# Optimization experiments

Measured on AMD Instinct MI355X. Metric: run time of the kernel, lower is better.

## Reference

```python
import jax, jax.numpy as jnp
import numpy as np

N_NODES = 100000
N_EDGES = 3200000
NUM_FEATURES = 512
LATENT_DIM = 64
HIDDEN = 2 * LATENT_DIM


def gcn_conv(x, src, dst, deg_inv_sqrt, W, b, n_nodes):
    # GCNConv: out = D^{-1/2} (A+I) D^{-1/2} X W + b  (transform first, then aggregate)
    h = x @ W  # [N, out]
    norm = deg_inv_sqrt[src] * deg_inv_sqrt[dst]  # [E]
    msg = h[src] * norm[:, None]  # gather + scale
    out = jax.ops.segment_sum(msg, dst, num_segments=n_nodes)
    return out + b


def setup_inputs() -> dict:
    key = jax.random.key(0)
    ks = jax.random.split(key, 8)
    features = jax.random.normal(ks[0], (N_NODES, NUM_FEATURES), dtype=jnp.float32)
    edge_index = jax.random.randint(ks[1], (2, N_EDGES), 0, N_NODES, dtype=jnp.int64)
    # Glorot-ish params
    W1 = jax.random.normal(ks[2], (NUM_FEATURES, HIDDEN), dtype=jnp.float32) / np.sqrt(NUM_FEATURES)
    b1 = jnp.zeros((HIDDEN,), dtype=jnp.float32)
    Wm = jax.random.normal(ks[3], (HIDDEN, LATENT_DIM), dtype=jnp.float32) / np.sqrt(HIDDEN)
    bm = jnp.zeros((LATENT_DIM,), dtype=jnp.float32)
    Wv = jax.random.normal(ks[4], (HIDDEN, LATENT_DIM), dtype=jnp.float32) / np.sqrt(HIDDEN)
    bv = jnp.zeros((LATENT_DIM,), dtype=jnp.float32)
    return {"features": features, "edge_index": edge_index,
            "W1": W1, "b1": b1, "Wm": Wm, "bm": bm, "Wv": Wv, "bv": bv}


def reference(features, edge_index, W1, b1, Wm, bm, Wv, bv):
    n = features.shape[0]
    loop = jnp.arange(n, dtype=edge_index.dtype)
    src = jnp.concatenate([edge_index[0], loop])  # add self-loops
    dst = jnp.concatenate([edge_index[1], loop])
    deg = jax.ops.segment_sum(jnp.ones_like(dst, dtype=features.dtype), dst, num_segments=n)
    deg_inv_sqrt = jnp.where(deg > 0, jax.lax.rsqrt(deg), 0.0)

    h = jax.nn.relu(gcn_conv(features, src, dst, deg_inv_sqrt, W1, b1, n))
    mean = gcn_conv(h, src, dst, deg_inv_sqrt, Wm, bm, n)
    var = gcn_conv(h, src, dst, deg_inv_sqrt, Wv, bv, n)
    return (mean, var)
```

## Files before the change

kernel.cpp:

```cpp
#include <hip/hip_runtime.h>

#define N_FEAT 512
#define HID 128
#define LAT 64

#define NB 98
#define BSHIFT 10
#define BS 1024
#define CAP 34816
#define CHUNK 4096

__device__ __forceinline__ unsigned short f2bf(float f) {
    unsigned u = __float_as_uint(f);
    return (unsigned short)((u + 0x7FFFu + ((u >> 16) & 1u)) >> 16);
}
__device__ __forceinline__ float bf2f(unsigned short h) {
    return __uint_as_float(((unsigned)h) << 16);
}

typedef __attribute__((ext_vector_type(8))) short bf16x8;
typedef __attribute__((ext_vector_type(4))) float f32x4;
typedef __attribute__((ext_vector_type(8))) unsigned short u16x8;

__global__ __launch_bounds__(256) void bin_kernel(const int* __restrict__ src,
                                                  const int* __restrict__ dst,
                                                  int* __restrict__ gcursor,
                                                  uint2* __restrict__ binned, int E) {
    __shared__ int hist[NB];
    __shared__ int basel[NB];
    __shared__ int gbase[NB];
    __shared__ int cursor[NB];
    __shared__ uint2 staged[CHUNK];
    int tid = threadIdx.x;
    int e0 = blockIdx.x * CHUNK;
    int nE = min(CHUNK, E - e0);
    if (nE <= 0) return;
    for (int i = tid; i < NB; i += 256) hist[i] = 0;
    __syncthreads();
    for (int i = tid; i < nE; i += 256) {
        int d = dst[e0 + i];
        atomicAdd(&hist[d >> BSHIFT], 1);
    }
    __syncthreads();
    if (tid < NB) basel[tid] = hist[tid];
    __syncthreads();
    for (int off = 1; off < NB; off <<= 1) {
        int x = (tid >= off && tid < NB) ? basel[tid - off] : 0;
        __syncthreads();
        if (tid < NB) basel[tid] += x;
        __syncthreads();
    }
    if (tid < NB) {
        int c = hist[tid];
        basel[tid] -= c;
        gbase[tid] = (c > 0) ? atomicAdd(&gcursor[tid], c) : 0;
        cursor[tid] = basel[tid];
    }
    __syncthreads();
    for (int i = tid; i < nE; i += 256) {
        int s = src[e0 + i];
        int d = dst[e0 + i];
        int b = d >> BSHIFT;
        int pos = atomicAdd(&cursor[b], 1);
        staged[pos] = make_uint2((unsigned)s, (unsigned)d);
    }
    __syncthreads();
    for (int i = tid; i < nE; i += 256) {
        uint2 e = staged[i];
        int b = (int)(e.y >> BSHIFT);
        int ofs = gbase[b] + (i - basel[b]);
        if (ofs < CAP) binned[(size_t)b * CAP + ofs] = e;
    }
}

__global__ __launch_bounds__(1024) void build_kernel(const uint2* __restrict__ binned,
                                                     const int* __restrict__ gcursor,
                                                     int* __restrict__ counts,
                                                     float* __restrict__ dis,
                                                     int* __restrict__ offsets,
                                                     int* __restrict__ pairs, int N) {
    __shared__ int nh[BS];
    __shared__ int pref[BS];
    int b = blockIdx.x;
    int tid = threadIdx.x;
    int nEdges = min(gcursor[b], CAP);
    const uint2* rgn = binned + (size_t)b * CAP;
    nh[tid] = 0;
    __syncthreads();
    for (int i = tid; i < nEdges; i += 1024)
        atomicAdd(&nh[rgn[i].y & (BS - 1)], 1);
    __syncthreads();
    int v = nh[tid];
    pref[tid] = v;
    __syncthreads();
    for (int off = 1; off < BS; off <<= 1) {
        int x = (tid >= off) ? pref[tid - off] : 0;
        __syncthreads();
        pref[tid] += x;
        __syncthreads();
    }
    int excl = pref[tid] - v;
    int node = (b << BSHIFT) + tid;
    if (node < N) {
        counts[node] = v;
        dis[node] = rsqrtf((float)(v + 1));
        offsets[node] = b * CAP + excl;
    }
    __syncthreads();
    nh[tid] = b * CAP + excl;
    __syncthreads();
    for (int i = tid; i < nEdges; i += 1024) {
        uint2 e = rgn[i];
        int pos = atomicAdd(&nh[e.y & (BS - 1)], 1);
        pairs[pos] = (int)e.x;
    }
}

__global__ __launch_bounds__(256) void wsplit_kernel(const float* __restrict__ W,
                                                     unsigned short* __restrict__ WhT,
                                                     unsigned short* __restrict__ WlT) {
    int i = blockIdx.x * 256 + threadIdx.x;
    if (i >= N_FEAT * HID) return;
    int k = i >> 7;
    int n = i & 127;
    float w = W[i];
    unsigned short h = f2bf(w);
    float r = w - bf2f(h);
    WhT[(size_t)n * N_FEAT + k] = h;
    WlT[(size_t)n * N_FEAT + k] = f2bf(r);
}

__global__ __launch_bounds__(256) void wsplit2_kernel(const float* __restrict__ Wm,
                                                      const float* __restrict__ Wv,
                                                      unsigned short* __restrict__ WhT2,
                                                      unsigned short* __restrict__ WlT2) {
    int i = blockIdx.x * 256 + threadIdx.x;
    if (i >= HID * HID) return;
    int k = i >> 7;
    int n = i & 127;
    float w = (n < 64) ? Wm[(size_t)k * LAT + n] : Wv[(size_t)k * LAT + (n - 64)];
    unsigned short h = f2bf(w);
    float r = w - bf2f(h);
    WhT2[(size_t)n * HID + k] = h;
    WlT2[(size_t)n * HID + k] = f2bf(r);
}

#define GM 128
#define GK 32
#define LDA 40

__global__ __launch_bounds__(256) void gemm1_mfma(const float* __restrict__ X,
                                                  const unsigned short* __restrict__ WhT,
                                                  const unsigned short* __restrict__ WlT,
                                                  const float* __restrict__ dis,
                                                  unsigned short* __restrict__ Tb, int M) {
    __shared__ unsigned short Ah[GM][LDA];
    __shared__ unsigned short Al[GM][LDA];
    __shared__ unsigned short Bh[HID][LDA];
    __shared__ unsigned short Bl[HID][LDA];

    int tid = threadIdx.x;
    int row = tid >> 1;
    int c0 = (tid & 1) * 16;

    int row_g = blockIdx.x * GM + row;
    if (row_g > M - 1) row_g = M - 1;
    const float* xbase = X + (size_t)row_g * N_FEAT;
    const unsigned short* whb = WhT + (size_t)row * N_FEAT;
    const unsigned short* wlb = WlT + (size_t)row * N_FEAT;

    int wid = tid >> 6, lane = tid & 63;
    int wm = wid >> 1, wn = wid & 1;
    int lm = lane & 15;
    int lk8 = (lane >> 4) * 8;

    f32x4 acc[4][4];
    #pragma unroll
    for (int i = 0; i < 4; ++i)
        #pragma unroll
        for (int j = 0; j < 4; ++j) acc[i][j] = (f32x4){0.f, 0.f, 0.f, 0.f};

    float4 xv0 = *(const float4*)(xbase + c0);
    float4 xv1 = *(const float4*)(xbase + c0 + 4);
    float4 xv2 = *(const float4*)(xbase + c0 + 8);
    float4 xv3 = *(const float4*)(xbase + c0 + 12);
    uint4 bhv0 = *(const uint4*)(whb + c0);
    uint4 bhv1 = *(const uint4*)(whb + c0 + 8);
    uint4 blv0 = *(const uint4*)(wlb + c0);
    uint4 blv1 = *(const uint4*)(wlb + c0 + 8);

    for (int k0 = 0; k0 < N_FEAT; k0 += GK) {
        __syncthreads();
        {
            float xs[16] = {xv0.x, xv0.y, xv0.z, xv0.w, xv1.x, xv1.y, xv1.z, xv1.w,
                            xv2.x, xv2.y, xv2.z, xv2.w, xv3.x, xv3.y, xv3.z, xv3.w};
            unsigned short* arow = &Ah[row][c0];
            unsigned short* lrow = &Al[row][c0];
            #pragma unroll
            for (int j = 0; j < 16; j += 2) {
                unsigned short h0 = f2bf(xs[j]);
                unsigned short h1 = f2bf(xs[j + 1]);
                float r0 = xs[j] - bf2f(h0);
                float r1 = xs[j + 1] - bf2f(h1);
                *(unsigned*)&arow[j] = (unsigned)h0 | ((unsigned)h1 << 16);
                *(unsigned*)&lrow[j] = (unsigned)f2bf(r0) | ((unsigned)f2bf(r1) << 16);
            }
            *(uint4*)&Bh[row][c0]     = bhv0;
            *(uint4*)&Bh[row][c0 + 8] = bhv1;
            *(uint4*)&Bl[row][c0]     = blv0;
            *(uint4*)&Bl[row][c0 + 8] = blv1;
        }
        __syncthreads();
        if (k0 + GK < N_FEAT) {
            const float* xp = xbase + k0 + GK + c0;
            xv0 = *(const float4*)(xp);
            xv1 = *(const float4*)(xp + 4);
            xv2 = *(const float4*)(xp + 8);
            xv3 = *(const float4*)(xp + 12);
            bhv0 = *(const uint4*)(whb + k0 + GK + c0);
            bhv1 = *(const uint4*)(whb + k0 + GK + c0 + 8);
            blv0 = *(const uint4*)(wlb + k0 + GK + c0);
            blv1 = *(const uint4*)(wlb + k0 + GK + c0 + 8);
        }
        bf16x8 ah[4], al[4], bh[4], bl[4];
        #pragma unroll
        for (int i = 0; i < 4; ++i) {
            ah[i] = *(const bf16x8*)&Ah[wm * 64 + i * 16 + lm][lk8];
            al[i] = *(const bf16x8*)&Al[wm * 64 + i * 16 + lm][lk8];
            bh[i] = *(const bf16x8*)&Bh[wn * 64 + i * 16 + lm][lk8];
            bl[i] = *(const bf16x8*)&Bl[wn * 64 + i * 16 + lm][lk8];
        }
        #pragma unroll
        for (int i = 0; i < 4; ++i)
            #pragma unroll
            for (int j = 0; j < 4; ++j) {
                acc[i][j] = __builtin_amdgcn_mfma_f32_16x16x32_bf16(ah[i], bh[j], acc[i][j], 0, 0, 0);
                acc[i][j] = __builtin_amdgcn_mfma_f32_16x16x32_bf16(al[i], bh[j], acc[i][j], 0, 0, 0);
                acc[i][j] = __builtin_amdgcn_mfma_f32_16x16x32_bf16(ah[i], bl[j], acc[i][j], 0, 0, 0);
            }
    }

    int orow0 = blockIdx.x * GM + wm * 64 + (lane >> 4) * 4;
    int ocol0 = wn * 64 + lm;
    #pragma unroll
    for (int i = 0; i < 4; ++i)
        #pragma unroll
        for (int r = 0; r < 4; ++r) {
            int orow = orow0 + i * 16 + r;
            if (orow < M) {
                float dr = dis[orow];
                #pragma unroll
                for (int j = 0; j < 4; ++j)
                    Tb[(size_t)orow * HID + ocol0 + j * 16] = f2bf(dr * acc[i][j][r]);
            }
        }
}

__global__ __launch_bounds__(256) void gemm2_mfma(const unsigned short* __restrict__ Gh,
                                                  const unsigned short* __restrict__ Gl,
                                                  const unsigned short* __restrict__ WhT2,
                                                  const unsigned short* __restrict__ WlT2,
                                                  const float* __restrict__ bm,
                                                  const float* __restrict__ bv,
                                                  float* __restrict__ outm,
                                                  float* __restrict__ outv, int M) {
    __shared__ unsigned short Ah[GM][LDA];
    __shared__ unsigned short Al[GM][LDA];
    __shared__ unsigned short Bh[HID][LDA];
    __shared__ unsigned short Bl[HID][LDA];

    int tid = threadIdx.x;
    int row = tid >> 1;
    int c0 = (tid & 1) * 16;

    int row_g = blockIdx.x * GM + row;
    if (row_g > M - 1) row_g = M - 1;
    const unsigned short* ghb = Gh + (size_t)row_g * HID;
    const unsigned short* glb = Gl + (size_t)row_g * HID;
    const unsigned short* whb = WhT2 + (size_t)row * HID;
    const unsigned short* wlb = WlT2 + (size_t)row * HID;

    int wid = tid >> 6, lane = tid & 63;
    int wm = wid >> 1, wn = wid & 1;
    int lm = lane & 15;
    int lk8 = (lane >> 4) * 8;

    f32x4 acc[4][4];
    #pragma unroll
    for (int i = 0; i < 4; ++i)
        #pragma unroll
        for (int j = 0; j < 4; ++j) acc[i][j] = (f32x4){0.f, 0.f, 0.f, 0.f};

    uint4 ahv0 = *(const uint4*)(ghb + c0);
    uint4 ahv1 = *(const uint4*)(ghb + c0 + 8);
    uint4 alv0 = *(const uint4*)(glb + c0);
    uint4 alv1 = *(const uint4*)(glb + c0 + 8);
    uint4 bhv0 = *(const uint4*)(whb + c0);
    uint4 bhv1 = *(const uint4*)(whb + c0 + 8);
    uint4 blv0 = *(const uint4*)(wlb + c0);
    uint4 blv1 = *(const uint4*)(wlb + c0 + 8);

    for (int k0 = 0; k0 < HID; k0 += GK) {
        __syncthreads();
        *(uint4*)&Ah[row][c0]     = ahv0;
        *(uint4*)&Ah[row][c0 + 8] = ahv1;
        *(uint4*)&Al[row][c0]     = alv0;
        *(uint4*)&Al[row][c0 + 8] = alv1;
        *(uint4*)&Bh[row][c0]     = bhv0;
        *(uint4*)&Bh[row][c0 + 8] = bhv1;
        *(uint4*)&Bl[row][c0]     = blv0;
        *(uint4*)&Bl[row][c0 + 8] = blv1;
        __syncthreads();
        if (k0 + GK < HID) {
            ahv0 = *(const uint4*)(ghb + k0 + GK + c0);
            ahv1 = *(const uint4*)(ghb + k0 + GK + c0 + 8);
            alv0 = *(const uint4*)(glb + k0 + GK + c0);
            alv1 = *(const uint4*)(glb + k0 + GK + c0 + 8);
            bhv0 = *(const uint4*)(whb + k0 + GK + c0);
            bhv1 = *(const uint4*)(whb + k0 + GK + c0 + 8);
            blv0 = *(const uint4*)(wlb + k0 + GK + c0);
            blv1 = *(const uint4*)(wlb + k0 + GK + c0 + 8);
        }
        bf16x8 ah[4], al[4], bh[4], bl[4];
        #pragma unroll
        for (int i = 0; i < 4; ++i) {
            ah[i] = *(const bf16x8*)&Ah[wm * 64 + i * 16 + lm][lk8];
            al[i] = *(const bf16x8*)&Al[wm * 64 + i * 16 + lm][lk8];
            bh[i] = *(const bf16x8*)&Bh[wn * 64 + i * 16 + lm][lk8];
            bl[i] = *(const bf16x8*)&Bl[wn * 64 + i * 16 + lm][lk8];
        }
        #pragma unroll
        for (int i = 0; i < 4; ++i)
            #pragma unroll
            for (int j = 0; j < 4; ++j) {
                acc[i][j] = __builtin_amdgcn_mfma_f32_16x16x32_bf16(ah[i], bh[j], acc[i][j], 0, 0, 0);
                acc[i][j] = __builtin_amdgcn_mfma_f32_16x16x32_bf16(al[i], bh[j], acc[i][j], 0, 0, 0);
                acc[i][j] = __builtin_amdgcn_mfma_f32_16x16x32_bf16(ah[i], bl[j], acc[i][j], 0, 0, 0);
            }
    }

    int orow0 = blockIdx.x * GM + wm * 64 + (lane >> 4) * 4;
    #pragma unroll
    for (int j = 0; j < 4; ++j) {
        int col = wn * 64 + j * 16 + lm;
        float bb = (col < 64) ? bm[col] : bv[col - 64];
        float* optr = (col < 64) ? (outm + col) : (outv + (col - 64));
        #pragma unroll
        for (int i = 0; i < 4; ++i)
            #pragma unroll
            for (int r = 0; r < 4; ++r) {
                int orow = orow0 + i * 16 + r;
                if (orow < M) optr[(size_t)orow * LAT] = acc[i][j][r] + bb;
            }
    }
}

#define AD 12
template <bool RELU_BIAS, bool SPLIT_OUT>
__global__ __launch_bounds__(256) void agg_kernel(const unsigned short* __restrict__ Tb,
                                                  const int* __restrict__ pairs,
                                                  const int* __restrict__ offsets,
                                                  const int* __restrict__ counts,
                                                  const float* __restrict__ dis,
                                                  const float* __restrict__ bias,
                                                  unsigned short* __restrict__ out_h,
                                                  unsigned short* __restrict__ out_l, int n) {
    int tid = threadIdx.x;
    int q = tid >> 4;
    int lane = tid & 15;
    int i = blockIdx.x * 16 + q;
    if (i >= n) return;
    float di = dis[i];
    int beg = offsets[i];
    int cnt = counts[i];
    const int* ep = pairs + beg;
    u16x8 self = ((const u16x8*)(Tb + (size_t)i * HID))[lane];
    float acc[8];
    #pragma unroll
    for (int e = 0; e < 8; ++e) acc[e] = bf2f(self[e]);
    if (cnt > 0) {
        int cm1 = cnt - 1;
        int s[AD];
        #pragma unroll
        for (int u = 0; u < AD; ++u)
            s[u] = (u <= cm1) ? ep[min(u, cm1)] : n;
        for (int j = 0; j < cnt; j += AD) {
            u16x8 v[AD];
            #pragma unroll
            for (int u = 0; u < AD; ++u)
                v[u] = ((const u16x8*)(Tb + (size_t)s[u] * HID))[lane];
            int jn = j + AD;
            int sN[AD];
            #pragma unroll
            for (int u = 0; u < AD; ++u)
                sN[u] = (jn + u <= cm1) ? ep[min(jn + u, cm1)] : n;
            #pragma unroll
            for (int u = 0; u < AD; ++u)
                #pragma unroll
                for (int e = 0; e < 8; ++e)
                    acc[e] += bf2f(v[u][e]);
            #pragma unroll
            for (int u = 0; u < AD; ++u) s[u] = sN[u];
        }
    }
    if (RELU_BIAS) {
        float4 bv0 = *(const float4*)(bias + lane * 8);
        float4 bv1 = *(const float4*)(bias + lane * 8 + 4);
        float bb[8] = {bv0.x, bv0.y, bv0.z, bv0.w, bv1.x, bv1.y, bv1.z, bv1.w};
        #pragma unroll
        for (int e = 0; e < 8; ++e) {
            float t = fmaxf(di * acc[e] + bb[e], 0.f);
            acc[e] = di * t;
        }
    } else {
        #pragma unroll
        for (int e = 0; e < 8; ++e) acc[e] *= di;
    }
    if (!SPLIT_OUT) {
        u16x8 o;
        #pragma unroll
        for (int e = 0; e < 8; ++e) o[e] = f2bf(acc[e]);
        ((u16x8*)(out_h + (size_t)i * HID))[lane] = o;
    } else {
        u16x8 oh, ol;
        #pragma unroll
        for (int e = 0; e < 8; ++e) {
            unsigned short hh = f2bf(acc[e]);
            oh[e] = hh;
            ol[e] = f2bf(acc[e] - bf2f(hh));
        }
        ((u16x8*)(out_h + (size_t)i * HID))[lane] = oh;
        ((u16x8*)(out_l + (size_t)i * HID))[lane] = ol;
    }
}

extern "C" void kernel_launch(void* const* d_in, const int* in_sizes, int n_in,
                              void* d_out, int out_size, void* d_ws, size_t ws_size,
                              hipStream_t stream) {
    const float* X  = (const float*)d_in[0];
    const int* edge = (const int*)d_in[1];
    const float* W1 = (const float*)d_in[2];
    const float* b1 = (const float*)d_in[3];
    const float* Wm = (const float*)d_in[4];
    const float* bm = (const float*)d_in[5];
    const float* Wv = (const float*)d_in[6];
    const float* bv = (const float*)d_in[7];

    int N = in_sizes[0] / N_FEAT;
    int E = in_sizes[1] / 2;
    const int* srcp = edge;
    const int* dstp = edge + E;

    char* w = (char*)d_ws;
    size_t off = 0;
    auto alloc = [&](size_t bytes) -> void* {
        void* p = w + off;
        off = (off + bytes + 511) & ~(size_t)511;
        return p;
    };
    float* dis    = (float*)alloc((size_t)N * 4);
    int* counts   = (int*)alloc((size_t)N * 4);
    int* offsets  = (int*)alloc((size_t)N * 4);
    int* gcursor  = (int*)alloc((size_t)NB * 4);
    int* pairs    = (int*)alloc((size_t)NB * CAP * 4);
    unsigned short* tb = (unsigned short*)alloc((size_t)(N + 1) * HID * 2);
    unsigned short* hb = (unsigned short*)alloc((size_t)(N + 1) * HID * 2);
    unsigned short* whT = (unsigned short*)alloc((size_t)N_FEAT * HID * 2);
    unsigned short* wlT = (unsigned short*)alloc((size_t)N_FEAT * HID * 2);
    unsigned short* whT2 = (unsigned short*)alloc((size_t)HID * HID * 2);
    unsigned short* wlT2 = (unsigned short*)alloc((size_t)HID * HID * 2);
    unsigned short* gh = (unsigned short*)alloc((size_t)N * HID * 2);
    unsigned short* gl = (unsigned short*)alloc((size_t)N * HID * 2);
    uint2* binned = (uint2*)gh;

    hipMemsetAsync(gcursor, 0, (size_t)NB * 4, stream);
    hipMemsetAsync(tb + (size_t)N * HID, 0, (size_t)HID * 2, stream);
    hipMemsetAsync(hb + (size_t)N * HID, 0, (size_t)HID * 2, stream);
    int nChunks = (E + CHUNK - 1) / CHUNK;
    bin_kernel<<<nChunks, 256, 0, stream>>>(srcp, dstp, gcursor, binned, E);
    build_kernel<<<NB, 1024, 0, stream>>>(binned, gcursor, counts, dis, offsets, pairs, N);

    wsplit_kernel<<<(N_FEAT * HID + 255) / 256, 256, 0, stream>>>(W1, whT, wlT);
    wsplit2_kernel<<<(HID * HID + 255) / 256, 256, 0, stream>>>(Wm, Wv, whT2, wlT2);
    gemm1_mfma<<<(N + GM - 1) / GM, 256, 0, stream>>>(X, whT, wlT, dis, tb, N);
    agg_kernel<true, false><<<(N + 15) / 16, 256, 0, stream>>>(tb, pairs, offsets, counts, dis, b1, hb, nullptr, N);
    agg_kernel<false, true><<<(N + 15) / 16, 256, 0, stream>>>(hb, pairs, offsets, counts, dis, nullptr, gh, gl, N);

    float* outm = (float*)d_out;
    float* outv = outm + (size_t)N * LAT;
    gemm2_mfma<<<(N + GM - 1) / GM, 256, 0, stream>>>(gh, gl, whT2, wlT2, bm, bv, outm, outv, N);
}
```

Baseline: 687.6 us.

## Fuse second-layer aggregation with mean/var GEMM in one kernel

Fuses the second aggregation pass with the 128x128 output GEMM. Each block aggregates 16 nodes into shared memory in fp32, splits them into bf16 hi/lo on the fly, and runs MFMA against the split weights loaded straight from global memory. This drops the gh/gl intermediate write and read (about 100MB) and one kernel launch. In exchange the GEMM tile is small and re-reads weights per block. The binned scratch buffer is moved to tb, so the memsets of the padding rows are placed after the build step.

```diff
diff --git a/kernel.cpp b/kernel.cpp
--- a/kernel.cpp
+++ b/kernel.cpp
@@ -256,115 +256,14 @@
         }
 }
 
-__global__ __launch_bounds__(256) void gemm2_mfma(const unsigned short* __restrict__ Gh,
-                                                  const unsigned short* __restrict__ Gl,
-                                                  const unsigned short* __restrict__ WhT2,
-                                                  const unsigned short* __restrict__ WlT2,
-                                                  const float* __restrict__ bm,
-                                                  const float* __restrict__ bv,
-                                                  float* __restrict__ outm,
-                                                  float* __restrict__ outv, int M) {
-    __shared__ unsigned short Ah[GM][LDA];
-    __shared__ unsigned short Al[GM][LDA];
-    __shared__ unsigned short Bh[HID][LDA];
-    __shared__ unsigned short Bl[HID][LDA];
-
-    int tid = threadIdx.x;
-    int row = tid >> 1;
-    int c0 = (tid & 1) * 16;
-
-    int row_g = blockIdx.x * GM + row;
-    if (row_g > M - 1) row_g = M - 1;
-    const unsigned short* ghb = Gh + (size_t)row_g * HID;
-    const unsigned short* glb = Gl + (size_t)row_g * HID;
-    const unsigned short* whb = WhT2 + (size_t)row * HID;
-    const unsigned short* wlb = WlT2 + (size_t)row * HID;
-
-    int wid = tid >> 6, lane = tid & 63;
-    int wm = wid >> 1, wn = wid & 1;
-    int lm = lane & 15;
-    int lk8 = (lane >> 4) * 8;
-
-    f32x4 acc[4][4];
-    #pragma unroll
-    for (int i = 0; i < 4; ++i)
-        #pragma unroll
-        for (int j = 0; j < 4; ++j) acc[i][j] = (f32x4){0.f, 0.f, 0.f, 0.f};
-
-    uint4 ahv0 = *(const uint4*)(ghb + c0);
-    uint4 ahv1 = *(const uint4*)(ghb + c0 + 8);
-    uint4 alv0 = *(const uint4*)(glb + c0);
-    uint4 alv1 = *(const uint4*)(glb + c0 + 8);
-    uint4 bhv0 = *(const uint4*)(whb + c0);
-    uint4 bhv1 = *(const uint4*)(whb + c0 + 8);
-    uint4 blv0 = *(const uint4*)(wlb + c0);
-    uint4 blv1 = *(const uint4*)(wlb + c0 + 8);
-
-    for (int k0 = 0; k0 < HID; k0 += GK) {
-        __syncthreads();
-        *(uint4*)&Ah[row][c0]     = ahv0;
-        *(uint4*)&Ah[row][c0 + 8] = ahv1;
-        *(uint4*)&Al[row][c0]     = alv0;
-        *(uint4*)&Al[row][c0 + 8] = alv1;
-        *(uint4*)&Bh[row][c0]     = bhv0;
-        *(uint4*)&Bh[row][c0 + 8] = bhv1;
-        *(uint4*)&Bl[row][c0]     = blv0;
-        *(uint4*)&Bl[row][c0 + 8] = blv1;
-        __syncthreads();
-        if (k0 + GK < HID) {
-            ahv0 = *(const uint4*)(ghb + k0 + GK + c0);
-            ahv1 = *(const uint4*)(ghb + k0 + GK + c0 + 8);
-            alv0 = *(const uint4*)(glb + k0 + GK + c0);
-            alv1 = *(const uint4*)(glb + k0 + GK + c0 + 8);
-            bhv0 = *(const uint4*)(whb + k0 + GK + c0);
-            bhv1 = *(const uint4*)(whb + k0 + GK + c0 + 8);
-            blv0 = *(const uint4*)(wlb + k0 + GK + c0);
-            blv1 = *(const uint4*)(wlb + k0 + GK + c0 + 8);
-        }
-        bf16x8 ah[4], al[4], bh[4], bl[4];
-        #pragma unroll
-        for (int i = 0; i < 4; ++i) {
-            ah[i] = *(const bf16x8*)&Ah[wm * 64 + i * 16 + lm][lk8];
-            al[i] = *(const bf16x8*)&Al[wm * 64 + i * 16 + lm][lk8];
-            bh[i] = *(const bf16x8*)&Bh[wn * 64 + i * 16 + lm][lk8];
-            bl[i] = *(const bf16x8*)&Bl[wn * 64 + i * 16 + lm][lk8];
-        }
-        #pragma unroll
-        for (int i = 0; i < 4; ++i)
-            #pragma unroll
-            for (int j = 0; j < 4; ++j) {
-                acc[i][j] = __builtin_amdgcn_mfma_f32_16x16x32_bf16(ah[i], bh[j], acc[i][j], 0, 0, 0);
-                acc[i][j] = __builtin_amdgcn_mfma_f32_16x16x32_bf16(al[i], bh[j], acc[i][j], 0, 0, 0);
-                acc[i][j] = __builtin_amdgcn_mfma_f32_16x16x32_bf16(ah[i], bl[j], acc[i][j], 0, 0, 0);
-            }
-    }
-
-    int orow0 = blockIdx.x * GM + wm * 64 + (lane >> 4) * 4;
-    #pragma unroll
-    for (int j = 0; j < 4; ++j) {
-        int col = wn * 64 + j * 16 + lm;
-        float bb = (col < 64) ? bm[col] : bv[col - 64];
-        float* optr = (col < 64) ? (outm + col) : (outv + (col - 64));
-        #pragma unroll
-        for (int i = 0; i < 4; ++i)
-            #pragma unroll
-            for (int r = 0; r < 4; ++r) {
-                int orow = orow0 + i * 16 + r;
-                if (orow < M) optr[(size_t)orow * LAT] = acc[i][j][r] + bb;
-            }
-    }
-}
-
 #define AD 12
-template <bool RELU_BIAS, bool SPLIT_OUT>
-__global__ __launch_bounds__(256) void agg_kernel(const unsigned short* __restrict__ Tb,
-                                                  const int* __restrict__ pairs,
-                                                  const int* __restrict__ offsets,
-                                                  const int* __restrict__ counts,
-                                                  const float* __restrict__ dis,
-                                                  const float* __restrict__ bias,
-                                                  unsigned short* __restrict__ out_h,
-                                                  unsigned short* __restrict__ out_l, int n) {
+__global__ __launch_bounds__(256) void agg1_kernel(const unsigned short* __restrict__ Tb,
+                                                   const int* __restrict__ pairs,
+                                                   const int* __restrict__ offsets,
+                                                   const int* __restrict__ counts,
+                                                   const float* __restrict__ dis,
+                                                   const float* __restrict__ bias,
+                                                   unsigned short* __restrict__ out, int n) {
     int tid = threadIdx.x;
     int q = tid >> 4;
     int lane = tid & 15;
@@ -403,34 +302,118 @@
             for (int u = 0; u < AD; ++u) s[u] = sN[u];
         }
     }
-    if (RELU_BIAS) {
-        float4 bv0 = *(const float4*)(bias + lane * 8);
-        float4 bv1 = *(const float4*)(bias + lane * 8 + 4);
-        float bb[8] = {bv0.x, bv0.y, bv0.z, bv0.w, bv1.x, bv1.y, bv1.z, bv1.w};
+    float4 bv0 = *(const float4*)(bias + lane * 8);
+    float4 bv1 = *(const float4*)(bias + lane * 8 + 4);
+    float bb[8] = {bv0.x, bv0.y, bv0.z, bv0.w, bv1.x, bv1.y, bv1.z, bv1.w};
+    u16x8 o;
+    #pragma unroll
+    for (int e = 0; e < 8; ++e) {
+        float t = fmaxf(di * acc[e] + bb[e], 0.f);
+        o[e] = f2bf(di * t);
+    }
+    ((u16x8*)(out + (size_t)i * HID))[lane] = o;
+}
+
+__global__ __launch_bounds__(256) void agg2_fused(const unsigned short* __restrict__ Tb,
+                                                  const int* __restrict__ pairs,
+                                                  const int* __restrict__ offsets,
+                                                  const int* __restrict__ counts,
+                                                  const float* __restrict__ dis,
+                                                  const unsigned short* __restrict__ WhT2,
+                                                  const unsigned short* __restrict__ WlT2,
+                                                  const float* __restrict__ bm,
+                                                  const float* __restrict__ bv,
+                                                  float* __restrict__ outm,
+                                                  float* __restrict__ outv, int n) {
+    __shared__ float Ga[16][HID + 4];
+    int tid = threadIdx.x;
+    int q = tid >> 4;
+    int lane16 = tid & 15;
+    int i = blockIdx.x * 16 + q;
+    bool alive = (i < n);
+    float di = alive ? dis[i] : 0.f;
+    int beg = alive ? offsets[i] : 0;
+    int cnt = alive ? counts[i] : 0;
+    const int* ep = pairs + beg;
+    float acc[8];
+    if (alive) {
+        u16x8 self = ((const u16x8*)(Tb + (size_t)i * HID))[lane16];
+        #pragma unroll
+        for (int e = 0; e < 8; ++e) acc[e] = bf2f(self[e]);
+    } else {
+        #pragma unroll
+        for (int e = 0; e < 8; ++e) acc[e] = 0.f;
+    }
+    if (cnt > 0) {
+        int cm1 = cnt - 1;
+        int s[AD];
+        #pragma unroll
+        for (int u = 0; u < AD; ++u)
+            s[u] = (u <= cm1) ? ep[min(u, cm1)] : n;
+        for (int j = 0; j < cnt; j += AD) {
+            u16x8 v[AD];
+            #pragma unroll
+            for (int u = 0; u < AD; ++u)
+                v[u] = ((const u16x8*)(Tb + (size_t)s[u] * HID))[lane16];
+            int jn = j + AD;
+            int sN[AD];
+            #pragma unroll
+            for (int u = 0; u < AD; ++u)
+                sN[u] = (jn + u <= cm1) ? ep[min(jn + u, cm1)] : n;
+            #pragma unroll
+            for (int u = 0; u < AD; ++u)
+                #pragma unroll
+                for (int e = 0; e < 8; ++e)
+                    acc[e] += bf2f(v[u][e]);
+            #pragma unroll
+            for (int u = 0; u < AD; ++u) s[u] = sN[u];
+        }
+    }
+    {
+        float4 g0 = {di * acc[0], di * acc[1], di * acc[2], di * acc[3]};
+        float4 g1 = {di * acc[4], di * acc[5], di * acc[6], di * acc[7]};
+        *(float4*)&Ga[q][lane16 * 8]     = g0;
+        *(float4*)&Ga[q][lane16 * 8 + 4] = g1;
+    }
+    __syncthreads();
+    int wv = tid >> 6;
+    int lane = tid & 63;
+    int lm = lane & 15;
+    int lk8 = (lane >> 4) * 8;
+    f32x4 oacc[2];
+    oacc[0] = (f32x4){0.f, 0.f, 0.f, 0.f};
+    oacc[1] = (f32x4){0.f, 0.f, 0.f, 0.f};
+    #pragma unroll
+    for (int k0 = 0; k0 < HID; k0 += GK) {
+        bf16x8 ah, al;
         #pragma unroll
         for (int e = 0; e < 8; ++e) {
-            float t = fmaxf(di * acc[e] + bb[e], 0.f);
-            acc[e] = di * t;
-        }
-    } else {
-        #pragma unroll
-        for (int e = 0; e < 8; ++e) acc[e] *= di;
-    }
-    if (!SPLIT_OUT) {
-        u16x8 o;
-        #pragma unroll
-        for (int e = 0; e < 8; ++e) o[e] = f2bf(acc[e]);
-        ((u16x8*)(out_h + (size_t)i * HID))[lane] = o;
-    } else {
-        u16x8 oh, ol;
-        #pragma unroll
-        for (int e = 0; e < 8; ++e) {
-            unsigned short hh = f2bf(acc[e]);
-            oh[e] = hh;
-            ol[e] = f2bf(acc[e] - bf2f(hh));
-        }
-        ((u16x8*)(out_h + (size_t)i * HID))[lane] = oh;
-        ((u16x8*)(out_l + (size_t)i * HID))[lane] = ol;
+            float x = Ga[lm][k0 + lk8 + e];
+            unsigned short hh = f2bf(x);
+            ah[e] = (short)hh;
+            al[e] = (short)f2bf(x - bf2f(hh));
+        }
+        #pragma unroll
+        for (int jt = 0; jt < 2; ++jt) {
+            size_t nrow = (size_t)(wv * 32 + jt * 16 + lm);
+            bf16x8 bh = *(const bf16x8*)(WhT2 + nrow * HID + k0 + lk8);
+            bf16x8 bl = *(const bf16x8*)(WlT2 + nrow * HID + k0 + lk8);
+            oacc[jt] = __builtin_amdgcn_mfma_f32_16x16x32_bf16(ah, bh, oacc[jt], 0, 0, 0);
+            oacc[jt] = __builtin_amdgcn_mfma_f32_16x16x32_bf16(al, bh, oacc[jt], 0, 0, 0);
+            oacc[jt] = __builtin_amdgcn_mfma_f32_16x16x32_bf16(ah, bl, oacc[jt], 0, 0, 0);
+        }
+    }
+    int nodeBase = blockIdx.x * 16 + (lane >> 4) * 4;
+    #pragma unroll
+    for (int jt = 0; jt < 2; ++jt) {
+        int col = wv * 32 + jt * 16 + lm;
+        float bb = (col < 64) ? bm[col] : bv[col - 64];
+        float* optr = (col < 64) ? (outm + col) : (outv + (col - 64));
+        #pragma unroll
+        for (int r = 0; r < 4; ++r) {
+            int node = nodeBase + r;
+            if (node < n) optr[(size_t)node * LAT] = oacc[jt][r] + bb;
+        }
     }
 }
 
@@ -469,24 +452,22 @@
     unsigned short* wlT = (unsigned short*)alloc((size_t)N_FEAT * HID * 2);
     unsigned short* whT2 = (unsigned short*)alloc((size_t)HID * HID * 2);
     unsigned short* wlT2 = (unsigned short*)alloc((size_t)HID * HID * 2);
-    unsigned short* gh = (unsigned short*)alloc((size_t)N * HID * 2);
-    unsigned short* gl = (unsigned short*)alloc((size_t)N * HID * 2);
-    uint2* binned = (uint2*)gh;
+    uint2* binned = (uint2*)tb;
 
     hipMemsetAsync(gcursor, 0, (size_t)NB * 4, stream);
-    hipMemsetAsync(tb + (size_t)N * HID, 0, (size_t)HID * 2, stream);
-    hipMemsetAsync(hb + (size_t)N * HID, 0, (size_t)HID * 2, stream);
     int nChunks = (E + CHUNK - 1) / CHUNK;
     bin_kernel<<<nChunks, 256, 0, stream>>>(srcp, dstp, gcursor, binned, E);
     build_kernel<<<NB, 1024, 0, stream>>>(binned, gcursor, counts, dis, offsets, pairs, N);
+    hipMemsetAsync(tb + (size_t)N * HID, 0, (size_t)HID * 2, stream);
+    hipMemsetAsync(hb + (size_t)N * HID, 0, (size_t)HID * 2, stream);
 
     wsplit_kernel<<<(N_FEAT * HID + 255) / 256, 256, 0, stream>>>(W1, whT, wlT);
     wsplit2_kernel<<<(HID * HID + 255) / 256, 256, 0, stream>>>(Wm, Wv, whT2, wlT2);
     gemm1_mfma<<<(N + GM - 1) / GM, 256, 0, stream>>>(X, whT, wlT, dis, tb, N);
-    agg_kernel<true, false><<<(N + 15) / 16, 256, 0, stream>>>(tb, pairs, offsets, counts, dis, b1, hb, nullptr, N);
-    agg_kernel<false, true><<<(N + 15) / 16, 256, 0, stream>>>(hb, pairs, offsets, counts, dis, nullptr, gh, gl, N);
+    agg1_kernel<<<(N + 15) / 16, 256, 0, stream>>>(tb, pairs, offsets, counts, dis, b1, hb, N);
 
     float* outm = (float*)d_out;
     float* outv = outm + (size_t)N * LAT;
-    gemm2_mfma<<<(N + GM - 1) / GM, 256, 0, stream>>>(gh, gl, whT2, wlT2, bm, bv, outm, outv, N);
-}
+    agg2_fused<<<(N + 15) / 16, 256, 0, stream>>>(hb, pairs, offsets, counts, dis,
+                                                  whT2, wlT2, bm, bv, outm, outv, N);
+}
```

New measurement: 662.0 us. 1.04x faster.
